# Optimization experiments

Hardware: AMD Instinct MI355X
Metric: run time of the kernel (lower is better)

Reference implementation:

```python
import jax, jax.numpy as jnp
import numpy as np

VOCAB, E, S, H, L = 32000, 1024, 2048, 16, 2
HS = E // H  # head_size = 64
EPS = 1e-5


def setup_inputs() -> dict:
    key = jax.random.key(0)
    ks = jax.random.split(key, 12)
    sc = 0.02
    inp = {
        "seq": jax.random.randint(ks[0], (S,), 0, VOCAB, dtype=jnp.int64)
        if jax.config.jax_enable_x64 else jax.random.randint(ks[0], (S,), 0, VOCAB, dtype=jnp.int32),
        "tok_emb": jax.random.normal(ks[1], (VOCAB, E), jnp.float32) * sc,
        "pos_emb": jax.random.normal(ks[2], (S, E), jnp.float32) * sc,
        "Wq": jax.random.normal(ks[3], (L, H, E, HS), jnp.float32) * sc,
        "Wk": jax.random.normal(ks[4], (L, H, E, HS), jnp.float32) * sc,
        "Wv": jax.random.normal(ks[5], (L, H, E, HS), jnp.float32) * sc,
        "Wr": jax.random.normal(ks[6], (L, E, E), jnp.float32) * sc,
        "br": jnp.zeros((L, E), jnp.float32),
        "W1": jax.random.normal(ks[7], (L, E, 4 * E), jnp.float32) * sc,
        "b1": jnp.zeros((L, 4 * E), jnp.float32),
        "W2": jax.random.normal(ks[8], (L, 4 * E, E), jnp.float32) * sc,
        "b2": jnp.zeros((L, E), jnp.float32),
        "ln_g": jnp.ones((L, E), jnp.float32),
        "ln_b": jnp.zeros((L, E), jnp.float32),
    }
    return inp


def _layer_norm(x, g, b):
    mu = jnp.mean(x, axis=-1, keepdims=True)
    var = jnp.mean(jnp.square(x - mu), axis=-1, keepdims=True)
    return (x - mu) * jax.lax.rsqrt(var + EPS) * g + b


def reference(seq, tok_emb, pos_emb, Wq, Wk, Wv, Wr, br, W1, b1, W2, b2, ln_g, ln_b):
    # embeddings: [S, E]
    x = tok_emb[seq] + pos_emb
    att_maps = []
    for l in range(L):
        # NOTE: the torch Block reuses the SAME LayerNorm instance twice per block.
        x = _layer_norm(x, ln_g[l], ln_b[l])
        # per-head projections: [H, S, HS]
        q = jnp.einsum('se,hed->hsd', x, Wq[l])
        k = jnp.einsum('se,hed->hsd', x, Wk[l])
        v = jnp.einsum('se,hed->hsd', x, Wv[l])
        # unmasked (encoder) attention, full [H, S, S] scores
        atts = jax.nn.softmax(jnp.einsum('hsd,htd->hst', q, k) / np.sqrt(HS), axis=-1)
        av = jnp.einsum('hst,htd->hsd', atts, v)  # [H, S, HS]
        cat = jnp.transpose(av, (1, 0, 2)).reshape(S, H * HS)  # concat heads -> [S, E]
        x = x + cat @ Wr[l] + br[l]
        x = _layer_norm(x, ln_g[l], ln_b[l])
        x = x + jax.nn.relu(x @ W1[l] + b1[l]) @ W2[l] + b2[l]
        att_maps.append(atts)
    return x, jnp.stack(att_maps)  # ([S,E], [L,H,S,S])
```

## Files before the change

### kernel.cpp

```cpp
#include <hip/hip_runtime.h>
#include <hip/hip_bf16.h>


constexpr int S_ = 2048;
constexpr int E_ = 1024;
constexpr int H_ = 16;
constexpr int HS_ = 64;
constexpr int L_ = 2;
constexpr int FF_ = 4096;

typedef __bf16 bf16;
typedef __bf16 bf16x8 __attribute__((ext_vector_type(8)));
typedef __bf16 bf16x4 __attribute__((ext_vector_type(4)));
typedef float f32x4 __attribute__((ext_vector_type(4)));

__device__ __forceinline__ void gld16(const void* g, const void* l) {
  __builtin_amdgcn_global_load_lds(
      (const __attribute__((address_space(1))) unsigned int*)g,
      (__attribute__((address_space(3))) unsigned int*)l, 16, 0, 0);
}

__global__ __launch_bounds__(256) void embed_ln_k(const int* __restrict__ seq,
                                                  const float* __restrict__ tok,
                                                  const float* __restrict__ pos,
                                                  const float* __restrict__ gw,
                                                  const float* __restrict__ bw,
                                                  float* __restrict__ x,
                                                  bf16* __restrict__ xb) {
  __shared__ float red[8];
  const int row = blockIdx.x, tid = threadIdx.x;
  const int t = seq[row];
  float4 v = ((const float4*)(tok + (long)t * E_))[tid];
  float4 p = ((const float4*)(pos + (long)row * E_))[tid];
  v.x += p.x; v.y += p.y; v.z += p.z; v.w += p.w;
  float s = v.x + v.y + v.z + v.w;
  float ss = v.x * v.x + v.y * v.y + v.z * v.z + v.w * v.w;
  for (int off = 32; off; off >>= 1) {
    s += __shfl_down(s, off);
    ss += __shfl_down(ss, off);
  }
  if ((tid & 63) == 0) { red[(tid >> 6) * 2] = s; red[(tid >> 6) * 2 + 1] = ss; }
  __syncthreads();
  if (tid == 0) {
    float S0 = 0, SS = 0;
    for (int i = 0; i < 4; ++i) { S0 += red[i * 2]; SS += red[i * 2 + 1]; }
    red[0] = S0; red[1] = SS;
  }
  __syncthreads();
  const float mu = red[0] * (1.f / E_);
  const float var = red[1] * (1.f / E_) - mu * mu;
  const float rs = rsqrtf(var + 1e-5f);
  float4 gv = ((const float4*)gw)[tid], bv = ((const float4*)bw)[tid];
  float4 o;
  o.x = (v.x - mu) * rs * gv.x + bv.x;
  o.y = (v.y - mu) * rs * gv.y + bv.y;
  o.z = (v.z - mu) * rs * gv.z + bv.z;
  o.w = (v.w - mu) * rs * gv.w + bv.w;
  ((float4*)(x + (long)row * E_))[tid] = o;
  bf16x4 ob;
  ob[0] = (__bf16)o.x; ob[1] = (__bf16)o.y; ob[2] = (__bf16)o.z; ob[3] = (__bf16)o.w;
  ((bf16x4*)(xb + (long)row * E_))[tid] = ob;
}

__global__ __launch_bounds__(256) void layernorm_k(float* __restrict__ x,
                                                   const float* __restrict__ gw,
                                                   const float* __restrict__ bw,
                                                   bf16* __restrict__ xb) {
  __shared__ float red[8];
  const int row = blockIdx.x, tid = threadIdx.x;
  float4 v = ((const float4*)(x + (long)row * E_))[tid];
  float s = v.x + v.y + v.z + v.w;
  float ss = v.x * v.x + v.y * v.y + v.z * v.z + v.w * v.w;
  for (int off = 32; off; off >>= 1) {
    s += __shfl_down(s, off);
    ss += __shfl_down(ss, off);
  }
  if ((tid & 63) == 0) { red[(tid >> 6) * 2] = s; red[(tid >> 6) * 2 + 1] = ss; }
  __syncthreads();
  if (tid == 0) {
    float S0 = 0, SS = 0;
    for (int i = 0; i < 4; ++i) { S0 += red[i * 2]; SS += red[i * 2 + 1]; }
    red[0] = S0; red[1] = SS;
  }
  __syncthreads();
  const float mu = red[0] * (1.f / E_);
  const float var = red[1] * (1.f / E_) - mu * mu;
  const float rs = rsqrtf(var + 1e-5f);
  float4 gv = ((const float4*)gw)[tid], bv = ((const float4*)bw)[tid];
  float4 o;
  o.x = (v.x - mu) * rs * gv.x + bv.x;
  o.y = (v.y - mu) * rs * gv.y + bv.y;
  o.z = (v.z - mu) * rs * gv.z + bv.z;
  o.w = (v.w - mu) * rs * gv.w + bv.w;
  ((float4*)(x + (long)row * E_))[tid] = o;
  bf16x4 ob;
  ob[0] = (__bf16)o.x; ob[1] = (__bf16)o.y; ob[2] = (__bf16)o.z; ob[3] = (__bf16)o.w;
  ((bf16x4*)(xb + (long)row * E_))[tid] = ob;
}

__global__ __launch_bounds__(256) void repack_k(const float* __restrict__ wq,
                                                const float* __restrict__ wk,
                                                const float* __restrict__ wv,
                                                const float* __restrict__ wr,
                                                const float* __restrict__ w1,
                                                const float* __restrict__ w2,
                                                bf16* __restrict__ qkvT,
                                                bf16* __restrict__ wrT,
                                                bf16* __restrict__ w1T,
                                                bf16* __restrict__ w2T) {
  __shared__ float t[32][33];
  const int tx = threadIdx.x, ty = threadIdx.y;
  const int bid = blockIdx.x;
  const float* src;
  bf16* dst;
  long ld_in, ld_out, r0, c0;
  if (bid < 3072) {
    const int j = bid >> 10;
    const int z = (bid & 1023) >> 6;
    const int rem = bid & 63;
    r0 = (rem >> 1) * 32;
    c0 = (rem & 1) * 32;
    const float* w = j == 0 ? wq : (j == 1 ? wk : wv);
    src = w + (long)z * E_ * HS_;
    dst = qkvT + (long)j * E_ * E_ + (long)z * HS_ * E_;
    ld_in = HS_; ld_out = E_;
  } else if (bid < 4096) {
    const int idx = bid - 3072;
    r0 = (idx >> 5) * 32; c0 = (idx & 31) * 32;
    src = wr; dst = wrT; ld_in = E_; ld_out = E_;
  } else if (bid < 8192) {
    const int idx = bid - 4096;
    r0 = (idx >> 7) * 32; c0 = (idx & 127) * 32;
    src = w1; dst = w1T; ld_in = FF_; ld_out = E_;
  } else {
    const int idx = bid - 8192;
    r0 = (idx >> 5) * 32; c0 = (idx & 31) * 32;
    src = w2; dst = w2T; ld_in = E_; ld_out = FF_;
  }
#pragma unroll
  for (int i = 0; i < 4; ++i)
    t[ty + 8 * i][tx] = src[(r0 + ty + 8 * i) * ld_in + c0 + tx];
  __syncthreads();
#pragma unroll
  for (int i = 0; i < 4; ++i)
    dst[(c0 + ty + 8 * i) * ld_out + r0 + tx] = (__bf16)t[tx][ty + 8 * i];
}

__global__ __launch_bounds__(256) void trans_b2b(const bf16* __restrict__ in,
                                                 bf16* __restrict__ out,
                                                 long ld_in, long ld_out) {
  __shared__ bf16 t[32][33];
  const int tx = threadIdx.x, ty = threadIdx.y;
  const long r0 = (long)blockIdx.x * 32, c0 = (long)blockIdx.y * 32;
#pragma unroll
  for (int i = 0; i < 4; ++i)
    t[ty + 8 * i][tx] = in[(r0 + ty + 8 * i) * ld_in + c0 + tx];
  __syncthreads();
#pragma unroll
  for (int i = 0; i < 4; ++i)
    out[(c0 + ty + 8 * i) * ld_out + r0 + tx] = t[tx][ty + 8 * i];
}

template <int WM, int WN>
__global__ __launch_bounds__(WM * WN * 64) void gemm_lds(
    const bf16* __restrict__ A, const bf16* __restrict__ B,
    long lda, long ldb, int K, int mtiles, float scale,
    const float* __restrict__ bias, const float* __restrict__ resid, int relu,
    float* __restrict__ Cf, long ldc, bf16* __restrict__ Cb, long ldcb) {
  constexpr int BM = WM * 64, BN = WN * 64, NW = WM * WN;
  constexpr int ABYTES = BM * 64;
  constexpr int BUFB = ABYTES + BN * 64;
  constexpr int NCH = BUFB / 1024;
  constexpr int CPT = NCH / NW;
  static_assert(CPT == 4 || CPT == 6, "unexpected CPT");
  __shared__ char smem[3 * BUFB];

  const int tid = threadIdx.x, wid = tid >> 6, lane = tid & 63;
  const int cpx = gridDim.x >> 3;
  const int bid = blockIdx.x;
  const int wg = (bid & 7) * cpx + (bid >> 3);
  const long m0 = (long)(wg % mtiles) * BM;
  const long n0 = (long)(wg / mtiles) * BN;

  const char* gsrc[CPT];
  int ldsbase[CPT];
#pragma unroll
  for (int i = 0; i < CPT; ++i) {
    const int c = wid + i * NW;
    const int s = c * 1024 + lane * 16;
    const bf16* base;
    int kb;
    if (s < ABYTES) {
      const int row = s >> 6;
      kb = (s ^ ((row & 3) << 4)) & 63;
      base = A + (m0 + row) * lda;
    } else {
      const int s2 = s - ABYTES;
      const int row = s2 >> 6;
      kb = (s2 ^ ((row & 3) << 4)) & 63;
      base = B + (n0 + row) * ldb;
    }
    gsrc[i] = (const char*)base + kb;
    ldsbase[i] = c * 1024;
  }

  const int fr = lane & 15, fg = lane >> 4;
  const int wm = wid % WM, wn = wid / WM;
  int aoff[4], boff[4];
#pragma unroll
  for (int t = 0; t < 4; ++t) {
    const int m = wm * 64 + t * 16 + fr;
    aoff[t] = m * 64 + ((16 * fg) ^ ((m & 3) << 4));
    const int n = wn * 64 + t * 16 + fr;
    boff[t] = ABYTES + n * 64 + ((16 * fg) ^ ((n & 3) << 4));
  }

  f32x4 acc[4][4];
#pragma unroll
  for (int i = 0; i < 4; ++i)
#pragma unroll
    for (int j = 0; j < 4; ++j) acc[i][j] = (f32x4){0.f, 0.f, 0.f, 0.f};

  const int nt = K >> 5;

  auto stage = [&](int tile, int buf) {
    const long koff = (long)tile * 64;
#pragma unroll
    for (int i = 0; i < CPT; ++i)
      gld16(gsrc[i] + koff, smem + buf * BUFB + ldsbase[i]);
  };

  stage(0, 0);
  stage(1, 1);

  int cur = 0;
  for (int t = 0; t < nt; ++t) {
    if (t < nt - 1) {
      if constexpr (CPT == 4) asm volatile("s_waitcnt vmcnt(4)" ::: "memory");
      else asm volatile("s_waitcnt vmcnt(6)" ::: "memory");
    } else {
      asm volatile("s_waitcnt vmcnt(0)" ::: "memory");
    }
    __builtin_amdgcn_s_barrier();
    if (t + 2 < nt) {
      int sb = cur + 2; if (sb >= 3) sb -= 3;
      stage(t + 2, sb);
    }
    const char* sbuf = smem + cur * BUFB;
    bf16x8 a[4], b[4];
#pragma unroll
    for (int i = 0; i < 4; ++i) a[i] = *(const bf16x8*)(sbuf + aoff[i]);
#pragma unroll
    for (int i = 0; i < 4; ++i) b[i] = *(const bf16x8*)(sbuf + boff[i]);
#pragma unroll
    for (int i = 0; i < 4; ++i)
#pragma unroll
      for (int j = 0; j < 4; ++j)
        acc[i][j] = __builtin_amdgcn_mfma_f32_16x16x32_bf16(a[i], b[j], acc[i][j], 0, 0, 0);
    cur = cur + 1; if (cur >= 3) cur -= 3;
  }

#pragma unroll
  for (int tm = 0; tm < 4; ++tm) {
#pragma unroll
    for (int tn = 0; tn < 4; ++tn) {
      const long col = n0 + wn * 64 + tn * 16 + fr;
#pragma unroll
      for (int i = 0; i < 4; ++i) {
        const long row = m0 + wm * 64 + tm * 16 + fg * 4 + i;
        float v = acc[tm][tn][i] * scale;
        if (bias) v += bias[col];
        if (relu) v = v > 0.f ? v : 0.f;
        if (resid) v += resid[row * ldc + col];
        if (Cf) Cf[row * ldc + col] = v;
        if (Cb) Cb[row * ldcb + col] = (__bf16)v;
      }
    }
  }
}

__global__ __launch_bounds__(256, 2) void attn_fused(
    const bf16* __restrict__ qkv,
    const bf16* __restrict__ vt,
    float* __restrict__ att,
    bf16* __restrict__ avb) {
  constexpr int QB = 128, KB = 128;
  constexpr int NKT = S_ / KB;
  constexpr float C2 = 0.1803368801111244f;
  __shared__ alignas(16) float plds[QB * KB];

  const int tid = threadIdx.x, lane = tid & 63, w = tid >> 6;
  const int fr = lane & 15, fg = lane >> 4;
  const int bid = blockIdx.x;
  const int wg = (bid & 7) * 32 + (bid >> 3);
  const int h = wg >> 4;
  const long q0 = (long)(wg & 15) * QB;
  const int qloc = w * 32;

  bf16x8 qf[2][2];
#pragma unroll
  for (int qnt = 0; qnt < 2; ++qnt)
#pragma unroll
    for (int k0 = 0; k0 < 2; ++k0)
      qf[qnt][k0] = *(const bf16x8*)(qkv + (q0 + qloc + qnt * 16 + fr) * (3 * E_) +
                                     h * HS_ + k0 * 32 + fg * 8);

  float l_[2] = {0.f, 0.f};

  for (int kt = 0; kt < NKT; ++kt) {
    const long t0 = (long)kt * KB;
    bf16x8 kf[8][2];
#pragma unroll
    for (int mt = 0; mt < 8; ++mt)
#pragma unroll
      for (int k0 = 0; k0 < 2; ++k0)
        kf[mt][k0] = *(const bf16x8*)(qkv + (t0 + mt * 16 + fr) * (3 * E_) +
                                      E_ + h * HS_ + k0 * 32 + fg * 8);
    f32x4 acc[8][2];
#pragma unroll
    for (int mt = 0; mt < 8; ++mt)
#pragma unroll
      for (int qnt = 0; qnt < 2; ++qnt) acc[mt][qnt] = (f32x4){0.f, 0.f, 0.f, 0.f};
#pragma unroll
    for (int k0 = 0; k0 < 2; ++k0)
#pragma unroll
      for (int mt = 0; mt < 8; ++mt)
#pragma unroll
        for (int qnt = 0; qnt < 2; ++qnt)
          acc[mt][qnt] = __builtin_amdgcn_mfma_f32_16x16x32_bf16(kf[mt][k0], qf[qnt][k0], acc[mt][qnt], 0, 0, 0);
#pragma unroll
    for (int qnt = 0; qnt < 2; ++qnt) {
      float sum = 0.f;
#pragma unroll
      for (int mt = 0; mt < 8; ++mt)
#pragma unroll
        for (int i = 0; i < 4; ++i) sum += __builtin_amdgcn_exp2f(acc[mt][qnt][i] * C2);
      l_[qnt] += sum;
    }
  }
#pragma unroll
  for (int qnt = 0; qnt < 2; ++qnt) {
    l_[qnt] += __shfl_xor(l_[qnt], 16);
    l_[qnt] += __shfl_xor(l_[qnt], 32);
  }
  const float invl[2] = {1.f / l_[0], 1.f / l_[1]};

  f32x4 ao[4][2];
#pragma unroll
  for (int d = 0; d < 4; ++d)
#pragma unroll
    for (int q = 0; q < 2; ++q) ao[d][q] = (f32x4){0.f, 0.f, 0.f, 0.f};

  for (int kt = 0; kt < NKT; ++kt) {
    const long t0 = (long)kt * KB;
    bf16x8 kf[8][2];
#pragma unroll
    for (int mt = 0; mt < 8; ++mt)
#pragma unroll
      for (int k0 = 0; k0 < 2; ++k0)
        kf[mt][k0] = *(const bf16x8*)(qkv + (t0 + mt * 16 + fr) * (3 * E_) +
                                      E_ + h * HS_ + k0 * 32 + fg * 8);
    f32x4 acc[8][2];
#pragma unroll
    for (int mt = 0; mt < 8; ++mt)
#pragma unroll
      for (int qnt = 0; qnt < 2; ++qnt) acc[mt][qnt] = (f32x4){0.f, 0.f, 0.f, 0.f};
#pragma unroll
    for (int k0 = 0; k0 < 2; ++k0)
#pragma unroll
      for (int mt = 0; mt < 8; ++mt)
#pragma unroll
        for (int qnt = 0; qnt < 2; ++qnt)
          acc[mt][qnt] = __builtin_amdgcn_mfma_f32_16x16x32_bf16(kf[mt][k0], qf[qnt][k0], acc[mt][qnt], 0, 0, 0);

#pragma unroll
    for (int qnt = 0; qnt < 2; ++qnt) {
      const int q = qloc + qnt * 16 + fr;
      const int swz = (q & 7) << 4;
#pragma unroll
      for (int mt = 0; mt < 8; ++mt) {
        f32x4 pv;
#pragma unroll
        for (int i = 0; i < 4; ++i)
          pv[i] = __builtin_amdgcn_exp2f(acc[mt][qnt][i] * C2) * invl[qnt];
        const int tb = (mt * 16 + fg * 4) * 4;
        *(f32x4*)((char*)plds + q * 512 + (tb ^ swz)) = pv;
      }
    }
    __syncthreads();

    {
      const int qq = tid >> 3, s8 = tid & 7;
#pragma unroll
      for (int rep = 0; rep < 4; ++rep) {
        const int q = qq + rep * 32;
        f32x4 v = *(const f32x4*)((char*)plds + q * 512 + ((s8 * 16) ^ ((q & 7) << 4)));
        __builtin_nontemporal_store(v, (f32x4*)(att + ((long)h * S_ + q0 + q) * S_ + t0 + s8 * 4));
      }
    }

#pragma unroll
    for (int k0 = 0; k0 < 4; ++k0) {
      bf16x8 bq[2];
#pragma unroll
      for (int qnt = 0; qnt < 2; ++qnt) {
        const int q = qloc + qnt * 16 + fr;
        const int swz = (q & 7) << 4;
        const int tb = k0 * 128 + fg * 32;
        f32x4 lo = *(const f32x4*)((char*)plds + q * 512 + (tb ^ swz));
        f32x4 hi = *(const f32x4*)((char*)plds + q * 512 + ((tb + 16) ^ swz));
        bf16x8 t;
#pragma unroll
        for (int j = 0; j < 4; ++j) { t[j] = (__bf16)lo[j]; t[4 + j] = (__bf16)hi[j]; }
        bq[qnt] = t;
      }
#pragma unroll
      for (int dmt = 0; dmt < 4; ++dmt) {
        bf16x8 av = *(const bf16x8*)(vt + (long)(h * HS_ + dmt * 16 + fr) * S_ +
                                     t0 + k0 * 32 + fg * 8);
#pragma unroll
        for (int qnt = 0; qnt < 2; ++qnt)
          ao[dmt][qnt] = __builtin_amdgcn_mfma_f32_16x16x32_bf16(av, bq[qnt], ao[dmt][qnt], 0, 0, 0);
      }
    }
    __syncthreads();
  }

#pragma unroll
  for (int qnt = 0; qnt < 2; ++qnt) {
    const int q = qloc + qnt * 16 + fr;
    const int swz = (q & 7) << 4;
#pragma unroll
    for (int dmt = 0; dmt < 4; ++dmt) {
      const int db = (dmt * 16 + fg * 4) * 4;
      *(f32x4*)((char*)plds + q * 256 + (db ^ swz)) = ao[dmt][qnt];
    }
  }
  __syncthreads();
  {
    const int q = tid >> 1, half = tid & 1;
    const int swz = (q & 7) << 4;
    bf16* dst = avb + (q0 + q) * E_ + h * HS_ + half * 32;
#pragma unroll
    for (int j = 0; j < 8; ++j) {
      f32x4 v = *(const f32x4*)((char*)plds + q * 256 + ((half * 128 + j * 16) ^ swz));
      bf16x4 o;
      o[0] = (__bf16)v[0]; o[1] = (__bf16)v[1]; o[2] = (__bf16)v[2]; o[3] = (__bf16)v[3];
      *(bf16x4*)(dst + j * 4) = o;
    }
  }
}

extern "C" void kernel_launch(void* const* d_in, const int* in_sizes, int n_in,
                              void* d_out, int out_size, void* d_ws, size_t ws_size,
                              hipStream_t stream) {
  const int* seq = (const int*)d_in[0];
  const float* tok_emb = (const float*)d_in[1];
  const float* pos_emb = (const float*)d_in[2];
  const float* Wq = (const float*)d_in[3];
  const float* Wk = (const float*)d_in[4];
  const float* Wv = (const float*)d_in[5];
  const float* Wr = (const float*)d_in[6];
  const float* br = (const float*)d_in[7];
  const float* W1 = (const float*)d_in[8];
  const float* b1 = (const float*)d_in[9];
  const float* W2 = (const float*)d_in[10];
  const float* b2 = (const float*)d_in[11];
  const float* ln_g = (const float*)d_in[12];
  const float* ln_b = (const float*)d_in[13];

  float* outx = (float*)d_out;
  float* att_all = outx + (long)S_ * E_;

  char* w = (char*)d_ws;
  auto alloc = [&](size_t bytes) {
    char* p = w;
    w += (bytes + 255) & ~(size_t)255;
    return p;
  };
  float* x = (float*)alloc((size_t)S_ * E_ * 4);
  bf16* xb = (bf16*)alloc((size_t)S_ * E_ * 2);
  bf16* qkvb = (bf16*)alloc((size_t)S_ * 3 * E_ * 2);
  bf16* vt = (bf16*)alloc((size_t)E_ * S_ * 2);
  bf16* avb = (bf16*)alloc((size_t)S_ * E_ * 2);
  bf16* hb = (bf16*)alloc((size_t)S_ * FF_ * 2);
  bf16* wqkvT = (bf16*)alloc((size_t)3 * E_ * E_ * 2);
  bf16* wrT = (bf16*)alloc((size_t)E_ * E_ * 2);
  bf16* w1T = (bf16*)alloc((size_t)E_ * FF_ * 2);
  bf16* w2T = (bf16*)alloc((size_t)E_ * FF_ * 2);
  (void)ws_size; (void)in_sizes; (void)n_in; (void)out_size;

  embed_ln_k<<<S_, 256, 0, stream>>>(seq, tok_emb, pos_emb, ln_g, ln_b, x, xb);

  for (int l = 0; l < L_; ++l) {
    repack_k<<<12288, dim3(32, 8, 1), 0, stream>>>(
        Wq + (long)l * H_ * E_ * HS_, Wk + (long)l * H_ * E_ * HS_,
        Wv + (long)l * H_ * E_ * HS_, Wr + (long)l * E_ * E_,
        W1 + (long)l * E_ * FF_, W2 + (long)l * FF_ * E_,
        wqkvT, wrT, w1T, w2T);

    if (l > 0)
      layernorm_k<<<S_, 256, 0, stream>>>(x, ln_g + (long)l * E_, ln_b + (long)l * E_, xb);

    gemm_lds<2, 2><<<dim3(16 * 24), 256, 0, stream>>>(
        xb, wqkvT, E_, E_, E_, 16, 1.f, nullptr, nullptr, 0,
        nullptr, 0, qkvb, 3 * E_);

    trans_b2b<<<dim3(S_ / 32, E_ / 32, 1), dim3(32, 8, 1), 0, stream>>>(
        qkvb + 2 * E_, vt, 3 * E_, S_);

    float* att_l = att_all + (long)l * H_ * S_ * S_;
    attn_fused<<<256, 256, 0, stream>>>(qkvb, vt, att_l, avb);

    gemm_lds<2, 1><<<dim3(16 * 16), 128, 0, stream>>>(
        avb, wrT, E_, E_, E_, 16, 1.f, br + (long)l * E_, x, 0,
        x, E_, nullptr, 0);

    layernorm_k<<<S_, 256, 0, stream>>>(x, ln_g + (long)l * E_, ln_b + (long)l * E_, xb);

    gemm_lds<2, 2><<<dim3(16 * 32), 256, 0, stream>>>(
        xb, w1T, E_, E_, E_, 16, 1.f, b1 + (long)l * FF_, nullptr, 1,
        nullptr, 0, hb, FF_);

    float* xdst = (l == L_ - 1) ? outx : x;
    gemm_lds<2, 1><<<dim3(16 * 16), 128, 0, stream>>>(
        hb, w2T, FF_, FF_, FF_, 16, 1.f, b2 + (long)l * E_, x, 0,
        xdst, E_, nullptr, 0);
  }
}
```

Baseline: 629.1 us.

## Replace multi-wave GEMM with single-wave 64x64 tile kernel without barriers

Replaces the templated multi-wave GEMM with a single-wavefront kernel that computes a 64x64 output tile. Because one wave now owns the whole LDS buffer, the inter-wave s_barrier is dropped and only vmcnt waits order the triple-buffered global-to-LDS loads. This removes barrier stalls and launches many more, smaller blocks for better occupancy and load balance. In exchange each block reuses less data from LDS, so global and L2 traffic for the A and B operands goes up.

```diff
diff --git a/kernel.cpp b/kernel.cpp
--- a/kernel.cpp
+++ b/kernel.cpp
@@ -161,58 +161,50 @@
     out[(c0 + ty + 8 * i) * ld_out + r0 + tx] = t[tx][ty + 8 * i];
 }
 
-template <int WM, int WN>
-__global__ __launch_bounds__(WM * WN * 64) void gemm_lds(
+__global__ __launch_bounds__(64) void gemm_w64(
     const bf16* __restrict__ A, const bf16* __restrict__ B,
     long lda, long ldb, int K, int mtiles, float scale,
     const float* __restrict__ bias, const float* __restrict__ resid, int relu,
     float* __restrict__ Cf, long ldc, bf16* __restrict__ Cb, long ldcb) {
-  constexpr int BM = WM * 64, BN = WN * 64, NW = WM * WN;
-  constexpr int ABYTES = BM * 64;
-  constexpr int BUFB = ABYTES + BN * 64;
-  constexpr int NCH = BUFB / 1024;
-  constexpr int CPT = NCH / NW;
-  static_assert(CPT == 4 || CPT == 6, "unexpected CPT");
+  constexpr int ABY = 4096;
+  constexpr int BUFB = 8192;
   __shared__ char smem[3 * BUFB];
 
-  const int tid = threadIdx.x, wid = tid >> 6, lane = tid & 63;
+  const int lane = threadIdx.x;
   const int cpx = gridDim.x >> 3;
   const int bid = blockIdx.x;
   const int wg = (bid & 7) * cpx + (bid >> 3);
-  const long m0 = (long)(wg % mtiles) * BM;
-  const long n0 = (long)(wg / mtiles) * BN;
-
-  const char* gsrc[CPT];
-  int ldsbase[CPT];
-#pragma unroll
-  for (int i = 0; i < CPT; ++i) {
-    const int c = wid + i * NW;
-    const int s = c * 1024 + lane * 16;
+  const long m0 = (long)(wg % mtiles) * 64;
+  const long n0 = (long)(wg / mtiles) * 64;
+
+  const char* gsrc[8];
+  int ldsbase[8];
+#pragma unroll
+  for (int i = 0; i < 8; ++i) {
+    const int s = i * 1024 + lane * 16;
     const bf16* base;
     int kb;
-    if (s < ABYTES) {
+    if (s < ABY) {
       const int row = s >> 6;
       kb = (s ^ ((row & 3) << 4)) & 63;
       base = A + (m0 + row) * lda;
     } else {
-      const int s2 = s - ABYTES;
+      const int s2 = s - ABY;
       const int row = s2 >> 6;
       kb = (s2 ^ ((row & 3) << 4)) & 63;
       base = B + (n0 + row) * ldb;
     }
     gsrc[i] = (const char*)base + kb;
-    ldsbase[i] = c * 1024;
+    ldsbase[i] = i * 1024;
   }
 
   const int fr = lane & 15, fg = lane >> 4;
-  const int wm = wid % WM, wn = wid / WM;
   int aoff[4], boff[4];
 #pragma unroll
   for (int t = 0; t < 4; ++t) {
-    const int m = wm * 64 + t * 16 + fr;
+    const int m = t * 16 + fr;
     aoff[t] = m * 64 + ((16 * fg) ^ ((m & 3) << 4));
-    const int n = wn * 64 + t * 16 + fr;
-    boff[t] = ABYTES + n * 64 + ((16 * fg) ^ ((n & 3) << 4));
+    boff[t] = ABY + m * 64 + ((16 * fg) ^ ((m & 3) << 4));
   }
 
   f32x4 acc[4][4];
@@ -226,7 +218,7 @@
   auto stage = [&](int tile, int buf) {
     const long koff = (long)tile * 64;
 #pragma unroll
-    for (int i = 0; i < CPT; ++i)
+    for (int i = 0; i < 8; ++i)
       gld16(gsrc[i] + koff, smem + buf * BUFB + ldsbase[i]);
   };
 
@@ -235,16 +227,14 @@
 
   int cur = 0;
   for (int t = 0; t < nt; ++t) {
-    if (t < nt - 1) {
-      if constexpr (CPT == 4) asm volatile("s_waitcnt vmcnt(4)" ::: "memory");
-      else asm volatile("s_waitcnt vmcnt(6)" ::: "memory");
-    } else {
-      asm volatile("s_waitcnt vmcnt(0)" ::: "memory");
-    }
-    __builtin_amdgcn_s_barrier();
     if (t + 2 < nt) {
       int sb = cur + 2; if (sb >= 3) sb -= 3;
       stage(t + 2, sb);
+      asm volatile("s_waitcnt vmcnt(16)" ::: "memory");
+    } else if (t + 1 < nt) {
+      asm volatile("s_waitcnt vmcnt(8)" ::: "memory");
+    } else {
+      asm volatile("s_waitcnt vmcnt(0)" ::: "memory");
     }
     const char* sbuf = smem + cur * BUFB;
     bf16x8 a[4], b[4];
@@ -264,10 +254,10 @@
   for (int tm = 0; tm < 4; ++tm) {
 #pragma unroll
     for (int tn = 0; tn < 4; ++tn) {
-      const long col = n0 + wn * 64 + tn * 16 + fr;
+      const long col = n0 + tn * 16 + fr;
 #pragma unroll
       for (int i = 0; i < 4; ++i) {
-        const long row = m0 + wm * 64 + tm * 16 + fg * 4 + i;
+        const long row = m0 + tm * 16 + fg * 4 + i;
         float v = acc[tm][tn][i] * scale;
         if (bias) v += bias[col];
         if (relu) v = v > 0.f ? v : 0.f;
@@ -502,8 +492,8 @@
     if (l > 0)
       layernorm_k<<<S_, 256, 0, stream>>>(x, ln_g + (long)l * E_, ln_b + (long)l * E_, xb);
 
-    gemm_lds<2, 2><<<dim3(16 * 24), 256, 0, stream>>>(
-        xb, wqkvT, E_, E_, E_, 16, 1.f, nullptr, nullptr, 0,
+    gemm_w64<<<32 * 48, 64, 0, stream>>>(
+        xb, wqkvT, E_, E_, E_, 32, 1.f, nullptr, nullptr, 0,
         nullptr, 0, qkvb, 3 * E_);
 
     trans_b2b<<<dim3(S_ / 32, E_ / 32, 1), dim3(32, 8, 1), 0, stream>>>(
@@ -512,19 +502,19 @@
     float* att_l = att_all + (long)l * H_ * S_ * S_;
     attn_fused<<<256, 256, 0, stream>>>(qkvb, vt, att_l, avb);
 
-    gemm_lds<2, 1><<<dim3(16 * 16), 128, 0, stream>>>(
-        avb, wrT, E_, E_, E_, 16, 1.f, br + (long)l * E_, x, 0,
+    gemm_w64<<<32 * 16, 64, 0, stream>>>(
+        avb, wrT, E_, E_, E_, 32, 1.f, br + (long)l * E_, x, 0,
         x, E_, nullptr, 0);
 
     layernorm_k<<<S_, 256, 0, stream>>>(x, ln_g + (long)l * E_, ln_b + (long)l * E_, xb);
 
-    gemm_lds<2, 2><<<dim3(16 * 32), 256, 0, stream>>>(
-        xb, w1T, E_, E_, E_, 16, 1.f, b1 + (long)l * FF_, nullptr, 1,
+    gemm_w64<<<32 * 64, 64, 0, stream>>>(
+        xb, w1T, E_, E_, E_, 32, 1.f, b1 + (long)l * FF_, nullptr, 1,
         nullptr, 0, hb, FF_);
 
     float* xdst = (l == L_ - 1) ? outx : x;
-    gemm_lds<2, 1><<<dim3(16 * 16), 128, 0, stream>>>(
-        hb, w2T, FF_, FF_, FF_, 16, 1.f, b2 + (long)l * E_, x, 0,
+    gemm_w64<<<32 * 16, 64, 0, stream>>>(
+        hb, w2T, FF_, FF_, FF_, 32, 1.f, b2 + (long)l * E_, x, 0,
         xdst, E_, nullptr, 0);
   }
 }
```

After: 674.2 us. 1.07x slower.

## Halve attention query tile, store probabilities directly, stage bf16 in LDS

Applied to the files above, without the earlier changes.

The attention kernel now processes 64 queries per block instead of 128, doubling the grid to 512 blocks so more CUs have work. Each wave handles one 16-query fragment. Probabilities are written straight from registers to global memory with nontemporal stores rather than being staged through fp32 LDS. Only bf16 copies go to a smaller swizzled LDS buffer for the PV MFMA, and the output epilogue writes bf16 directly without an LDS transpose. The trade-off is that K and V fragments are reloaded twice as often across blocks, and the direct att stores are less coalesced (16-byte chunks per lane, strided across rows).

```diff
diff --git a/kernel.cpp b/kernel.cpp
--- a/kernel.cpp
+++ b/kernel.cpp
@@ -284,28 +284,26 @@
     const bf16* __restrict__ vt,
     float* __restrict__ att,
     bf16* __restrict__ avb) {
-  constexpr int QB = 128, KB = 128;
+  constexpr int QB = 64, KB = 128;
   constexpr int NKT = S_ / KB;
   constexpr float C2 = 0.1803368801111244f;
-  __shared__ alignas(16) float plds[QB * KB];
+  __shared__ char plds[QB * 256];
 
   const int tid = threadIdx.x, lane = tid & 63, w = tid >> 6;
   const int fr = lane & 15, fg = lane >> 4;
   const int bid = blockIdx.x;
-  const int wg = (bid & 7) * 32 + (bid >> 3);
-  const int h = wg >> 4;
-  const long q0 = (long)(wg & 15) * QB;
-  const int qloc = w * 32;
-
-  bf16x8 qf[2][2];
-#pragma unroll
-  for (int qnt = 0; qnt < 2; ++qnt)
-#pragma unroll
-    for (int k0 = 0; k0 < 2; ++k0)
-      qf[qnt][k0] = *(const bf16x8*)(qkv + (q0 + qloc + qnt * 16 + fr) * (3 * E_) +
-                                     h * HS_ + k0 * 32 + fg * 8);
-
-  float l_[2] = {0.f, 0.f};
+  const int wg = (bid & 7) * 64 + (bid >> 3);
+  const int h = wg >> 5;
+  const long q0 = (long)(wg & 31) * QB;
+  const int q = w * 16 + fr;
+  const int swz = (q & 15) << 4;
+
+  bf16x8 qf[2];
+#pragma unroll
+  for (int k0 = 0; k0 < 2; ++k0)
+    qf[k0] = *(const bf16x8*)(qkv + (q0 + q) * (3 * E_) + h * HS_ + k0 * 32 + fg * 8);
+
+  float l_ = 0.f;
 
   for (int kt = 0; kt < NKT; ++kt) {
     const long t0 = (long)kt * KB;
@@ -316,40 +314,28 @@
       for (int k0 = 0; k0 < 2; ++k0)
         kf[mt][k0] = *(const bf16x8*)(qkv + (t0 + mt * 16 + fr) * (3 * E_) +
                                       E_ + h * HS_ + k0 * 32 + fg * 8);
-    f32x4 acc[8][2];
+    f32x4 acc[8];
+#pragma unroll
+    for (int mt = 0; mt < 8; ++mt) acc[mt] = (f32x4){0.f, 0.f, 0.f, 0.f};
+#pragma unroll
+    for (int k0 = 0; k0 < 2; ++k0)
+#pragma unroll
+      for (int mt = 0; mt < 8; ++mt)
+        acc[mt] = __builtin_amdgcn_mfma_f32_16x16x32_bf16(kf[mt][k0], qf[k0], acc[mt], 0, 0, 0);
+    float sum = 0.f;
 #pragma unroll
     for (int mt = 0; mt < 8; ++mt)
 #pragma unroll
-      for (int qnt = 0; qnt < 2; ++qnt) acc[mt][qnt] = (f32x4){0.f, 0.f, 0.f, 0.f};
-#pragma unroll
-    for (int k0 = 0; k0 < 2; ++k0)
-#pragma unroll
-      for (int mt = 0; mt < 8; ++mt)
-#pragma unroll
-        for (int qnt = 0; qnt < 2; ++qnt)
-          acc[mt][qnt] = __builtin_amdgcn_mfma_f32_16x16x32_bf16(kf[mt][k0], qf[qnt][k0], acc[mt][qnt], 0, 0, 0);
-#pragma unroll
-    for (int qnt = 0; qnt < 2; ++qnt) {
-      float sum = 0.f;
-#pragma unroll
-      for (int mt = 0; mt < 8; ++mt)
-#pragma unroll
-        for (int i = 0; i < 4; ++i) sum += __builtin_amdgcn_exp2f(acc[mt][qnt][i] * C2);
-      l_[qnt] += sum;
-    }
-  }
-#pragma unroll
-  for (int qnt = 0; qnt < 2; ++qnt) {
-    l_[qnt] += __shfl_xor(l_[qnt], 16);
-    l_[qnt] += __shfl_xor(l_[qnt], 32);
-  }
-  const float invl[2] = {1.f / l_[0], 1.f / l_[1]};
-
-  f32x4 ao[4][2];
-#pragma unroll
-  for (int d = 0; d < 4; ++d)
-#pragma unroll
-    for (int q = 0; q < 2; ++q) ao[d][q] = (f32x4){0.f, 0.f, 0.f, 0.f};
+      for (int i = 0; i < 4; ++i) sum += __builtin_amdgcn_exp2f(acc[mt][i] * C2);
+    l_ += sum;
+  }
+  l_ += __shfl_xor(l_, 16);
+  l_ += __shfl_xor(l_, 32);
+  const float invl = 1.f / l_;
+
+  f32x4 ao[4];
+#pragma unroll
+  for (int d = 0; d < 4; ++d) ao[d] = (f32x4){0.f, 0.f, 0.f, 0.f};
 
   for (int kt = 0; kt < NKT; ++kt) {
     const long t0 = (long)kt * KB;
@@ -360,94 +346,50 @@
       for (int k0 = 0; k0 < 2; ++k0)
         kf[mt][k0] = *(const bf16x8*)(qkv + (t0 + mt * 16 + fr) * (3 * E_) +
                                       E_ + h * HS_ + k0 * 32 + fg * 8);
-    f32x4 acc[8][2];
-#pragma unroll
-    for (int mt = 0; mt < 8; ++mt)
-#pragma unroll
-      for (int qnt = 0; qnt < 2; ++qnt) acc[mt][qnt] = (f32x4){0.f, 0.f, 0.f, 0.f};
+    f32x4 acc[8];
+#pragma unroll
+    for (int mt = 0; mt < 8; ++mt) acc[mt] = (f32x4){0.f, 0.f, 0.f, 0.f};
 #pragma unroll
     for (int k0 = 0; k0 < 2; ++k0)
 #pragma unroll
       for (int mt = 0; mt < 8; ++mt)
-#pragma unroll
-        for (int qnt = 0; qnt < 2; ++qnt)
-          acc[mt][qnt] = __builtin_amdgcn_mfma_f32_16x16x32_bf16(kf[mt][k0], qf[qnt][k0], acc[mt][qnt], 0, 0, 0);
-
-#pragma unroll
-    for (int qnt = 0; qnt < 2; ++qnt) {
-      const int q = qloc + qnt * 16 + fr;
-      const int swz = (q & 7) << 4;
-#pragma unroll
-      for (int mt = 0; mt < 8; ++mt) {
-        f32x4 pv;
-#pragma unroll
-        for (int i = 0; i < 4; ++i)
-          pv[i] = __builtin_amdgcn_exp2f(acc[mt][qnt][i] * C2) * invl[qnt];
-        const int tb = (mt * 16 + fg * 4) * 4;
-        *(f32x4*)((char*)plds + q * 512 + (tb ^ swz)) = pv;
-      }
+        acc[mt] = __builtin_amdgcn_mfma_f32_16x16x32_bf16(kf[mt][k0], qf[k0], acc[mt], 0, 0, 0);
+
+    float* arow = att + ((long)h * S_ + q0 + q) * S_ + t0;
+#pragma unroll
+    for (int mt = 0; mt < 8; ++mt) {
+      f32x4 pv;
+#pragma unroll
+      for (int i = 0; i < 4; ++i)
+        pv[i] = __builtin_amdgcn_exp2f(acc[mt][i] * C2) * invl;
+      __builtin_nontemporal_store(pv, (f32x4*)(arow + mt * 16 + fg * 4));
+      bf16x4 pb;
+      pb[0] = (__bf16)pv[0]; pb[1] = (__bf16)pv[1];
+      pb[2] = (__bf16)pv[2]; pb[3] = (__bf16)pv[3];
+      const int tb = (mt * 16 + fg * 4) * 2;
+      *(bf16x4*)(plds + q * 256 + ((tb & ~15) ^ swz) + (tb & 15)) = pb;
     }
     __syncthreads();
 
-    {
-      const int qq = tid >> 3, s8 = tid & 7;
-#pragma unroll
-      for (int rep = 0; rep < 4; ++rep) {
-        const int q = qq + rep * 32;
-        f32x4 v = *(const f32x4*)((char*)plds + q * 512 + ((s8 * 16) ^ ((q & 7) << 4)));
-        __builtin_nontemporal_store(v, (f32x4*)(att + ((long)h * S_ + q0 + q) * S_ + t0 + s8 * 4));
-      }
-    }
-
 #pragma unroll
     for (int k0 = 0; k0 < 4; ++k0) {
-      bf16x8 bq[2];
-#pragma unroll
-      for (int qnt = 0; qnt < 2; ++qnt) {
-        const int q = qloc + qnt * 16 + fr;
-        const int swz = (q & 7) << 4;
-        const int tb = k0 * 128 + fg * 32;
-        f32x4 lo = *(const f32x4*)((char*)plds + q * 512 + (tb ^ swz));
-        f32x4 hi = *(const f32x4*)((char*)plds + q * 512 + ((tb + 16) ^ swz));
-        bf16x8 t;
-#pragma unroll
-        for (int j = 0; j < 4; ++j) { t[j] = (__bf16)lo[j]; t[4 + j] = (__bf16)hi[j]; }
-        bq[qnt] = t;
-      }
+      const bf16x8 bq = *(const bf16x8*)(plds + q * 256 + ((k0 * 64 + fg * 16) ^ swz));
 #pragma unroll
       for (int dmt = 0; dmt < 4; ++dmt) {
         bf16x8 av = *(const bf16x8*)(vt + (long)(h * HS_ + dmt * 16 + fr) * S_ +
                                      t0 + k0 * 32 + fg * 8);
-#pragma unroll
-        for (int qnt = 0; qnt < 2; ++qnt)
-          ao[dmt][qnt] = __builtin_amdgcn_mfma_f32_16x16x32_bf16(av, bq[qnt], ao[dmt][qnt], 0, 0, 0);
+        ao[dmt] = __builtin_amdgcn_mfma_f32_16x16x32_bf16(av, bq, ao[dmt], 0, 0, 0);
       }
     }
     __syncthreads();
   }
 
 #pragma unroll
-  for (int qnt = 0; qnt < 2; ++qnt) {
-    const int q = qloc + qnt * 16 + fr;
-    const int swz = (q & 7) << 4;
-#pragma unroll
-    for (int dmt = 0; dmt < 4; ++dmt) {
-      const int db = (dmt * 16 + fg * 4) * 4;
-      *(f32x4*)((char*)plds + q * 256 + (db ^ swz)) = ao[dmt][qnt];
-    }
-  }
-  __syncthreads();
-  {
-    const int q = tid >> 1, half = tid & 1;
-    const int swz = (q & 7) << 4;
-    bf16* dst = avb + (q0 + q) * E_ + h * HS_ + half * 32;
-#pragma unroll
-    for (int j = 0; j < 8; ++j) {
-      f32x4 v = *(const f32x4*)((char*)plds + q * 256 + ((half * 128 + j * 16) ^ swz));
-      bf16x4 o;
-      o[0] = (__bf16)v[0]; o[1] = (__bf16)v[1]; o[2] = (__bf16)v[2]; o[3] = (__bf16)v[3];
-      *(bf16x4*)(dst + j * 4) = o;
-    }
+  for (int dmt = 0; dmt < 4; ++dmt) {
+    bf16x4 o;
+    o[0] = (__bf16)ao[dmt][0]; o[1] = (__bf16)ao[dmt][1];
+    o[2] = (__bf16)ao[dmt][2]; o[3] = (__bf16)ao[dmt][3];
+    *(bf16x4*)(avb + (q0 + q) * E_ + h * HS_ + dmt * 16 + fg * 4) = o;
   }
 }
 
@@ -510,7 +452,7 @@
         qkvb + 2 * E_, vt, 3 * E_, S_);
 
     float* att_l = att_all + (long)l * H_ * S_ * S_;
-    attn_fused<<<256, 256, 0, stream>>>(qkvb, vt, att_l, avb);
+    attn_fused<<<512, 256, 0, stream>>>(qkvb, vt, att_l, avb);
 
     gemm_lds<2, 1><<<dim3(16 * 16), 128, 0, stream>>>(
         avb, wrT, E_, E_, E_, 16, 1.f, br + (long)l * E_, x, 0,
```

Result: slower. 764.7 us (+21.6%).
